# Kernel optimization log

Hardware: AMD Instinct MI355X
Metric: run time of the kernel (lower is better)

The kernel has to match this reference:

```python
import jax, jax.numpy as jnp
import numpy as np
from jax import lax

M1, M2 = 16, 16  # retained Fourier modes per spatial dim


def _spectral_conv(x, w1, w2):
    # x: [B, C, H, W] real; w1/w2: [C, C, M1, M2, 2] (re, im)
    B, C, H, W = x.shape
    xf = jnp.fft.rfft2(x, norm='ortho')            # [B, C, H, W//2+1] complex
    w1c = w1[..., 0] + 1j * w1[..., 1]
    w2c = w2[..., 0] + 1j * w2[..., 1]
    top = jnp.einsum('bixy,ioxy->boxy', xf[:, :, :M1, :M2], w1c)
    bot = jnp.einsum('bixy,ioxy->boxy', xf[:, :, -M1:, :M2], w2c)
    of = jnp.zeros((B, C, H, W // 2 + 1), dtype=xf.dtype)
    of = of.at[:, :, :M1, :M2].set(top).at[:, :, -M1:, :M2].set(bot)
    return jnp.fft.irfft2(of, s=(H, W), norm='ortho')


def _fno_block(x, w1, w2, skip_w):
    # spectral conv + linear (1x1 conv, no bias) skip
    return _spectral_conv(x, w1, w2) + jnp.einsum('bixy,io->boxy', x, skip_w)


def setup_inputs() -> dict:
    key = jax.random.key(0)
    ks = jax.random.split(key, 6)
    B, T, C, H, W = 4, 8, 64, 64, 64
    scale = 1.0 / (C * C)
    return {
        'x': jax.random.normal(ks[0], (B, T, C, H, W), dtype=jnp.float32),
        'sw1': jax.random.normal(ks[1], (6, C, C, M1, M2, 2), dtype=jnp.float32) * scale,
        'sw2': jax.random.normal(ks[2], (6, C, C, M1, M2, 2), dtype=jnp.float32) * scale,
        'skw': jax.random.normal(ks[3], (6, C, C), dtype=jnp.float32) * 0.02,
        'gate_b': jax.random.normal(ks[4], (3,), dtype=jnp.float32),
        'bias_h': jax.random.normal(ks[5], (1,), dtype=jnp.float32),
    }


def reference(x, sw1, sw2, skw, gate_b, bias_h):
    B, T, C, H, W = x.shape

    def f(i, inp):
        return _fno_block(inp, sw1[i], sw2[i], skw[i])

    def cell(xt, h):
        z = jax.nn.sigmoid(f(0, xt) + f(1, h) + gate_b[0])
        r = jax.nn.sigmoid(f(2, xt) + f(3, h) + gate_b[1])
        h_hat = jax.nn.selu(f(4, xt) + f(5, r * h) + gate_b[2])
        return (1.0 - z) * h + z * h_hat

    def step(h, xt):
        h = cell(xt, h)
        return h, None

    h0 = jnp.full((B, C, H, W), bias_h[0], dtype=x.dtype)
    h_final, _ = lax.scan(step, h0, jnp.moveaxis(x, 1, 0))  # scan over T
    return h_final  # return_sequences=False -> final hidden state [B, C, H, W]
```

## Files before the change

### kernel.cpp

```cpp
#include <hip/hip_runtime.h>

#define BB_ 4
#define TT_ 8
#define CC_ 64
#define HW 4096
#define UMAP 1024
#define STEP 0.09817477042468103f

#define OFF_UXALL 0
#define OFF_UH    (OFF_UXALL + TT_*256*UMAP)
#define OFF_URH   (OFF_UH + 256*UMAP)
#define OFF_SX    (OFF_URH + 256*UMAP)
#define OFF_SPART (OFF_SX + 3*TT_*256*UMAP)
#define OFF_H     (OFF_SPART + 2*8*256*UMAP)
#define OFF_Z     (OFF_H + BB_*CC_*HW)
#define OFF_RH    (OFF_Z + BB_*CC_*HW)
#define OFF_PH    (OFF_RH + BB_*CC_*HW)

__global__ __launch_bounds__(256) void k_init(float* __restrict__ hb,
                                              float* __restrict__ Uh,
                                              const float* __restrict__ bias_h) {
    float v = bias_h[0];
    int blk = blockIdx.x;
    if (blk < 1024) {
        int idx = (blk * 256 + threadIdx.x) * 4;
        *(float4*)(hb + idx) = make_float4(v, v, v, v);
    } else {
        int map = blk - 1024;
        float4 z = make_float4(0.f, 0.f, 0.f, 0.f);
        if (threadIdx.x == 0) z.x = 64.f * v;
        *(float4*)(Uh + (size_t)map * UMAP + threadIdx.x * 4) = z;
    }
}

__device__ __forceinline__ void dft_stages(const float* __restrict__ su,
                                           float* __restrict__ FxR, float* __restrict__ FxI,
                                           float* __restrict__ dst) {
    int tid = threadIdx.x;
    int kx = tid & 15, yb = tid >> 4;
    float stc, sts;
    __sincosf(-STEP * (float)kx, &sts, &stc);
    float wr = 1.f, wi = 0.f;
    float aR[4] = {0, 0, 0, 0}, aI[4] = {0, 0, 0, 0};
    for (int x = 0; x < 64; x++) {
        #pragma unroll
        for (int j = 0; j < 4; j++) {
            float v = su[(yb + 16 * j) * 65 + x];
            aR[j] = fmaf(v, wr, aR[j]);
            aI[j] = fmaf(v, wi, aI[j]);
        }
        float t = wr * stc - wi * sts;
        wi = wr * sts + wi * stc;
        wr = t;
    }
    #pragma unroll
    for (int j = 0; j < 4; j++) {
        FxR[(yb + 16 * j) * 16 + kx] = aR[j];
        FxI[(yb + 16 * j) * 16 + kx] = aI[j];
    }
    __syncthreads();
    int kb = tid >> 4;
    float c0, s0, c1, s1;
    __sincosf(-STEP * (float)kb, &s0, &c0);
    __sincosf(-STEP * (float)(kb + 48), &s1, &c1);
    float w0r = 1, w0i = 0, w1r = 1, w1i = 0;
    float A0r = 0, A0i = 0, A1r = 0, A1i = 0;
    for (int y = 0; y < 64; y++) {
        float Fr = FxR[y * 16 + kx], Fi = FxI[y * 16 + kx];
        A0r = fmaf(Fr, w0r, A0r); A0r = fmaf(-Fi, w0i, A0r);
        A0i = fmaf(Fr, w0i, A0i); A0i = fmaf(Fi, w0r, A0i);
        A1r = fmaf(Fr, w1r, A1r); A1r = fmaf(-Fi, w1i, A1r);
        A1i = fmaf(Fr, w1i, A1i); A1i = fmaf(Fi, w1r, A1i);
        float t0 = w0r * c0 - w0i * s0; w0i = w0r * s0 + w0i * c0; w0r = t0;
        float t1 = w1r * c1 - w1i * s1; w1i = w1r * s1 + w1i * c1; w1r = t1;
    }
    const float sc = 1.f / 64.f;
    float2* d2 = (float2*)dst;
    d2[kb * 16 + kx]        = make_float2(A0r * sc, A0i * sc);
    d2[(kb + 16) * 16 + kx] = make_float2(A1r * sc, A1i * sc);
}

__device__ __forceinline__ void dft_stages_512(const float* __restrict__ su,
                                               float* __restrict__ FxR, float* __restrict__ FxI,
                                               float* __restrict__ dst) {
    int tid = threadIdx.x;
    int kx = tid & 15, yb = tid >> 4;
    float stc, sts;
    __sincosf(-STEP * (float)kx, &sts, &stc);
    float wr = 1.f, wi = 0.f;
    float aR[2] = {0, 0}, aI[2] = {0, 0};
    for (int x = 0; x < 64; x++) {
        #pragma unroll
        for (int j = 0; j < 2; j++) {
            float v = su[(yb + 32 * j) * 65 + x];
            aR[j] = fmaf(v, wr, aR[j]);
            aI[j] = fmaf(v, wi, aI[j]);
        }
        float t = wr * stc - wi * sts;
        wi = wr * sts + wi * stc;
        wr = t;
    }
    #pragma unroll
    for (int j = 0; j < 2; j++) {
        FxR[(yb + 32 * j) * 16 + kx] = aR[j];
        FxI[(yb + 32 * j) * 16 + kx] = aI[j];
    }
    __syncthreads();
    int kb = tid >> 4;
    int ky = (kb < 16) ? kb : kb + 32;
    float c0, s0;
    __sincosf(-STEP * (float)ky, &s0, &c0);
    float w0r = 1, w0i = 0, A0r = 0, A0i = 0;
    for (int y = 0; y < 64; y++) {
        float Fr = FxR[y * 16 + kx], Fi = FxI[y * 16 + kx];
        A0r = fmaf(Fr, w0r, A0r); A0r = fmaf(-Fi, w0i, A0r);
        A0i = fmaf(Fr, w0i, A0i); A0i = fmaf(Fi, w0r, A0i);
        float t0 = w0r * c0 - w0i * s0; w0i = w0r * s0 + w0i * c0; w0r = t0;
    }
    const float sc = 1.f / 64.f;
    ((float2*)dst)[kb * 16 + kx] = make_float2(A0r * sc, A0i * sc);
}

__global__ __launch_bounds__(256) void k_dft_x(const float* __restrict__ x,
                                               float* __restrict__ Uxall) {
    __shared__ float su[64 * 65];
    __shared__ float FxR[1024], FxI[1024];
    int blk = blockIdx.x;
    int t = blk >> 8, map = blk & 255;
    int b = map >> 6, c = map & 63;
    const float* src = x + (((size_t)b * TT_ + t) * CC_ + c) * HW;
    int tid = threadIdx.x;
    #pragma unroll
    for (int k = 0; k < 4; k++) {
        int off = k * 1024 + tid * 4;
        float4 v = *(const float4*)(src + off);
        int y = off >> 6, xx = off & 63;
        su[y * 65 + xx + 0] = v.x; su[y * 65 + xx + 1] = v.y;
        su[y * 65 + xx + 2] = v.z; su[y * 65 + xx + 3] = v.w;
    }
    __syncthreads();
    dft_stages(su, FxR, FxI, Uxall + ((size_t)t * 256 + map) * UMAP);
}

__device__ __forceinline__ void mix_load(const float2* __restrict__ W2,
                                         const float2* __restrict__ U2, int i,
                                         float2 w[4], float2 u[4]) {
    const float2* wp = W2 + (size_t)i * 16384;
    const float2* up = U2 + (size_t)i * 512;
    w[0] = wp[0]; w[1] = wp[256]; w[2] = wp[512]; w[3] = wp[768];
    u[0] = up[0]; u[1] = up[32768]; u[2] = up[65536]; u[3] = up[98304];
}

__device__ __forceinline__ void mix_fma(const float2 w[4], const float2 u[4],
                                        float aR[4][4], float aI[4][4]) {
    #pragma unroll
    for (int oo = 0; oo < 4; oo++)
        #pragma unroll
        for (int bb = 0; bb < 4; bb++) {
            aR[oo][bb] = fmaf(u[bb].x, w[oo].x, aR[oo][bb]);
            aR[oo][bb] = fmaf(-u[bb].y, w[oo].y, aR[oo][bb]);
            aI[oo][bb] = fmaf(u[bb].x, w[oo].y, aI[oo][bb]);
            aI[oo][bb] = fmaf(u[bb].y, w[oo].x, aI[oo][bb]);
        }
}

__device__ __forceinline__ void mix_accum(const float2* __restrict__ W2,
                                          const float2* __restrict__ U2,
                                          int niter, float aR[4][4], float aI[4][4])
{
    float2 wA[4], uA[4], wB[4], uB[4], wN[4], uN[4];
    mix_load(W2, U2, 0, wA, uA);
    mix_load(W2, U2, 1, wB, uB);
    for (int i = 0; i + 2 < niter; i += 2) {
        mix_load(W2, U2, i + 2, wN, uN);
        mix_fma(wA, uA, aR, aI);
        #pragma unroll
        for (int k = 0; k < 4; k++) { wA[k] = wN[k]; uA[k] = uN[k]; }
        mix_load(W2, U2, i + 3, wN, uN);
        mix_fma(wB, uB, aR, aI);
        #pragma unroll
        for (int k = 0; k < 4; k++) { wB[k] = wN[k]; uB[k] = uN[k]; }
    }
    mix_fma(wA, uA, aR, aI);
    mix_fma(wB, uB, aR, aI);
}

__global__ __launch_bounds__(512, 4) void k_mix_x(
    const float* __restrict__ Uxall,
    const float* __restrict__ sw1, const float* __restrict__ sw2,
    float* __restrict__ Sx)
{
    __shared__ float2 red2[16 * 256];
    int blk = blockIdx.x;
    int mq = blk & 3;
    int tp = (blk >> 2) & 3;
    int op = (blk >> 4) & 7;
    int half = (blk >> 7) & 1;
    int li = blk >> 8;
    int l = li * 2;
    int tid = threadIdx.x;
    int kc = tid >> 8;
    int r = tid & 255;
    int ml = r & 15, og1 = (r >> 4) & 1, t1 = (r >> 5) & 1, wq = r >> 6;
    int m = mq * 64 + wq * 16 + ml;
    int o0 = (op * 2 + og1) * 4;
    int t = tp * 2 + t1;
    const float2* wt = (const float2*)(half ? sw2 : sw1);
    const float2* W2 = wt + ((size_t)(l * 4096 + o0)) * 256 + m + (size_t)kc * 32 * 16384;
    const float2* U2 = (const float2*)Uxall + (size_t)t * 131072 + half * 256 + m
                       + (size_t)kc * 32 * 512;
    float aR[4][4], aI[4][4];
    #pragma unroll
    for (int oo = 0; oo < 4; oo++)
        #pragma unroll
        for (int b = 0; b < 4; b++) { aR[oo][b] = 0.f; aI[oo][b] = 0.f; }
    #pragma unroll 4
    for (int i = 0; i < 32; ++i) {
        float2 w[4], u[4];
        mix_load(W2, U2, i, w, u);
        mix_fma(w, u, aR, aI);
    }
    if (kc) {
        #pragma unroll
        for (int oo = 0; oo < 4; oo++)
            #pragma unroll
            for (int b = 0; b < 4; b++)
                red2[(oo * 4 + b) * 256 + r] = make_float2(aR[oo][b], aI[oo][b]);
    }
    __syncthreads();
    if (kc == 0) {
        float2* S2 = (float2*)Sx;
        #pragma unroll
        for (int oo = 0; oo < 4; oo++)
            #pragma unroll
            for (int b = 0; b < 4; b++) {
                float2 p = red2[(oo * 4 + b) * 256 + r];
                S2[((size_t)(li * 8 + t) * 256 + b * 64 + o0 + oo) * 512 + half * 256 + m]
                    = make_float2(aR[oo][b] + p.x, aI[oo][b] + p.y);
            }
    }
}

__device__ __forceinline__ void mix_body_h(int blk, int l0, int l1,
    const float* __restrict__ U,
    const float* __restrict__ sw1, const float* __restrict__ sw2,
    float* __restrict__ Spart)
{
    int og = blk & 15;
    int ic = (blk >> 4) & 7;
    int half = (blk >> 7) & 1;
    int g = (blk >> 8) & 1;
    int m = threadIdx.x;
    int o0 = og * 4, ib = ic * 8;
    int l = g ? l1 : l0;
    const float2* wt = (const float2*)(half ? sw2 : sw1);
    const float2* W2 = wt + (((size_t)l * 64 + ib) * 64 + o0) * 256 + m;
    const float2* U2 = (const float2*)U + (size_t)ib * 512 + half * 256 + m;
    float aR[4][4], aI[4][4];
    #pragma unroll
    for (int oo = 0; oo < 4; oo++)
        #pragma unroll
        for (int b = 0; b < 4; b++) { aR[oo][b] = 0.f; aI[oo][b] = 0.f; }
    mix_accum(W2, U2, 8, aR, aI);
    float2* S2 = (float2*)Spart;
    #pragma unroll
    for (int oo = 0; oo < 4; oo++)
        #pragma unroll
        for (int b = 0; b < 4; b++)
            S2[((size_t)(g * 8 + ic) * 256 + b * 64 + o0 + oo) * 512 + half * 256 + m]
                = make_float2(aR[oo][b], aI[oo][b]);
}

__device__ __forceinline__ void fma16(const float4 w, const float4 u, float acc[4][4]) {
    acc[0][0] = fmaf(u.x, w.x, acc[0][0]); acc[0][1] = fmaf(u.y, w.x, acc[0][1]);
    acc[0][2] = fmaf(u.z, w.x, acc[0][2]); acc[0][3] = fmaf(u.w, w.x, acc[0][3]);
    acc[1][0] = fmaf(u.x, w.y, acc[1][0]); acc[1][1] = fmaf(u.y, w.y, acc[1][1]);
    acc[1][2] = fmaf(u.z, w.y, acc[1][2]); acc[1][3] = fmaf(u.w, w.y, acc[1][3]);
    acc[2][0] = fmaf(u.x, w.z, acc[2][0]); acc[2][1] = fmaf(u.y, w.z, acc[2][1]);
    acc[2][2] = fmaf(u.z, w.z, acc[2][2]); acc[2][3] = fmaf(u.w, w.z, acc[2][3]);
    acc[3][0] = fmaf(u.x, w.w, acc[3][0]); acc[3][1] = fmaf(u.y, w.w, acc[3][1]);
    acc[3][2] = fmaf(u.z, w.w, acc[3][2]); acc[3][3] = fmaf(u.w, w.w, acc[3][3]);
}

__device__ __forceinline__ void skip_gemm(int rr, float* __restrict__ sW,
    const float* __restrict__ uA, long long bsA,
    const float* __restrict__ uB, long long bsB,
    const float* __restrict__ skw, int lA, int lB, float gb,
    float* __restrict__ out)
{
    int pxc = rr & 31, oh = (rr >> 5) & 1, b = rr >> 6;
    int tid = threadIdx.x;
    int ot = tid & 7, pt = tid >> 3;
    #pragma unroll
    for (int n = 0; n < 4; n++) {
        int idx = n * 1024 + tid * 4;
        int k = idx >> 5, oc = idx & 31;
        int p = k >> 6, i = k & 63;
        *(float4*)(sW + idx) =
            *(const float4*)(skw + (p ? lB : lA) * 4096 + i * 64 + oh * 32 + oc);
    }
    __syncthreads();
    float acc[4][4];
    #pragma unroll
    for (int oo = 0; oo < 4; oo++)
        #pragma unroll
        for (int q = 0; q < 4; q++) acc[oo][q] = 0.f;
    const float* pa = uA + (long long)b * bsA + pxc * 128 + pt * 4;
    const float* pb = uB + (long long)b * bsB + pxc * 128 + pt * 4;
    const float4* sW4 = (const float4*)sW;
    #pragma unroll 4
    for (int i = 0; i < 64; i++) {
        float4 ua = *(const float4*)(pa + (size_t)i * HW);
        float4 wa = sW4[i * 8 + ot];
        fma16(wa, ua, acc);
        float4 ub = *(const float4*)(pb + (size_t)i * HW);
        float4 wb = sW4[(64 + i) * 8 + ot];
        fma16(wb, ub, acc);
    }
    float* op = out + ((long long)(b * 64 + oh * 32 + ot * 4)) * HW + pxc * 128 + pt * 4;
    #pragma unroll
    for (int oo = 0; oo < 4; oo++) {
        float4 r = make_float4(acc[oo][0] + gb, acc[oo][1] + gb,
                               acc[oo][2] + gb, acc[oo][3] + gb);
        *(float4*)(op + (size_t)oo * HW) = r;
    }
}

__global__ __launch_bounds__(256) void k_front_zr(
    const float* __restrict__ Uh,
    const float* __restrict__ xt, const float* __restrict__ hb,
    const float* __restrict__ sw1, const float* __restrict__ sw2,
    const float* __restrict__ skw, const float* __restrict__ gate_b,
    float* __restrict__ Spart, float* __restrict__ zb, float* __restrict__ rhb)
{
    __shared__ float smem[4096];
    int blk = blockIdx.x;
    if (blk < 512) {
        mix_body_h(blk, 1, 3, Uh, sw1, sw2, Spart);
    } else {
        int r = blk - 512;
        int g = r >> 8;
        skip_gemm(r & 255, smem,
                  xt, (long long)TT_ * CC_ * HW, hb, (long long)CC_ * HW,
                  skw, g ? 2 : 0, g ? 3 : 1, gate_b[g], g ? rhb : zb);
    }
}

__global__ __launch_bounds__(256) void k_front_h(
    const float* __restrict__ Urh,
    const float* __restrict__ xt, const float* __restrict__ rhb,
    const float* __restrict__ sw1, const float* __restrict__ sw2,
    const float* __restrict__ skw, const float* __restrict__ gate_b,
    float* __restrict__ Spart, float* __restrict__ phb)
{
    __shared__ float smem[4096];
    int blk = blockIdx.x;
    if (blk < 256) {
        mix_body_h(blk, 5, 5, Urh, sw1, sw2, Spart);
    } else {
        int r = blk - 256;
        skip_gemm(r, smem,
                  xt, (long long)TT_ * CC_ * HW, rhb, (long long)CC_ * HW,
                  skw, 4, 5, gate_b[2], phb);
    }
}

__device__ __forceinline__ void idft_stage1_512(const float* __restrict__ SR,
                                                const float* __restrict__ SI,
                                                float* __restrict__ GR, float* __restrict__ GI)
{
    int tid = threadIdx.x;
    int kx = tid & 15, yb = tid >> 4;
    #pragma unroll
    for (int j = 0; j < 2; j++) {
        int y = yb + 32 * j;
        float stc, sts;
        __sincosf(STEP * (float)y, &sts, &stc);
        float ar = 0.f, ai = 0.f;
        float wr = 1.f, wi = 0.f;
        for (int k = 0; k < 16; k++) {
            float sr_ = SR[k * 16 + kx], si_ = SI[k * 16 + kx];
            ar = fmaf(sr_, wr, ar); ar = fmaf(-si_, wi, ar);
            ai = fmaf(sr_, wi, ai); ai = fmaf(si_, wr, ai);
            float t = wr * stc - wi * sts; wi = wr * sts + wi * stc; wr = t;
        }
        int q = (3 * y) & 3;
        float w2r = (q == 0) ? 1.f : ((q == 2) ? -1.f : 0.f);
        float w2i = (q == 1) ? 1.f : ((q == 3) ? -1.f : 0.f);
        for (int k = 16; k < 32; k++) {
            float sr_ = SR[k * 16 + kx], si_ = SI[k * 16 + kx];
            ar = fmaf(sr_, w2r, ar); ar = fmaf(-si_, w2i, ar);
            ai = fmaf(sr_, w2i, ai); ai = fmaf(si_, w2r, ai);
            float t = w2r * stc - w2i * sts; w2i = w2r * sts + w2i * stc; w2r = t;
        }
        GR[y * 16 + kx] = ar;
        GI[y * 16 + kx] = ai;
    }
}

__global__ __launch_bounds__(512) void k_back_zr(
    const float* __restrict__ Spart, const float* __restrict__ Sx, int t,
    float* __restrict__ zb, float* __restrict__ rhb,
    const float* __restrict__ hb, float* __restrict__ Urh)
{
    __shared__ float smem[6208];
    float* SR = smem;
    float* SI = smem + 512;
    float* GR = smem + 1024;
    float* GI = smem + 2048;
    int g = blockIdx.x >> 8;
    int map = blockIdx.x & 255;
    int tid = threadIdx.x;
    {
        float2 v = ((const float2*)Sx)[((size_t)(g * 8 + t) * 256 + map) * 512 + tid];
        float sr = v.x, si = v.y;
        const float2* base = (const float2*)Spart;
        #pragma unroll
        for (int ic = 0; ic < 8; ic++) {
            float2 p = base[((size_t)(g * 8 + ic) * 256 + map) * 512 + tid];
            sr += p.x; si += p.y;
        }
        SR[tid] = sr; SI[tid] = si;
    }
    __syncthreads();
    idft_stage1_512(SR, SI, GR, GI);
    __syncthreads();
    int x = tid & 63, ybase = tid >> 6;
    float cx, sx;
    __sincosf(STEP * (float)x, &sx, &cx);
    size_t mo = (size_t)map * HW;
    float rhv[8];
    #pragma unroll
    for (int j = 0; j < 8; j++) {
        int y = ybase + 8 * j;
        float acc = GR[y * 16];
        float wr = cx, wi = sx;
        #pragma unroll
        for (int k = 1; k < 16; k++) {
            acc = fmaf(2.f * GR[y * 16 + k], wr, acc);
            acc = fmaf(-2.f * GI[y * 16 + k], wi, acc);
            float t2 = wr * cx - wi * sx; wi = wr * sx + wi * cx; wr = t2;
        }
        float val = acc * (1.f / 64.f);
        int idx = y * 64 + x;
        if (g == 0) {
            float pre = val + zb[mo + idx];
            zb[mo + idx] = 1.f / (1.f + __expf(-pre));
        } else {
            float pre = val + rhb[mo + idx];
            float rr = 1.f / (1.f + __expf(-pre));
            float rh = rr * hb[mo + idx];
            rhb[mo + idx] = rh;
            rhv[j] = rh;
        }
    }
    if (g == 0) return;
    __syncthreads();
    float* su = smem;
    #pragma unroll
    for (int j = 0; j < 8; j++) {
        int y = ybase + 8 * j;
        su[y * 65 + x] = rhv[j];
    }
    __syncthreads();
    dft_stages_512(su, smem + 4160, smem + 5184, Urh + (size_t)map * UMAP);
}

__global__ __launch_bounds__(512) void k_back_h(
    const float* __restrict__ Spart, const float* __restrict__ Sx, int t,
    const float* __restrict__ zb, const float* __restrict__ phb,
    float* __restrict__ hb, float* __restrict__ Uh)
{
    __shared__ float smem[6208];
    float* SR = smem;
    float* SI = smem + 512;
    float* GR = smem + 1024;
    float* GI = smem + 2048;
    int map = blockIdx.x & 255;
    int tid = threadIdx.x;
    {
        float2 v = ((const float2*)Sx)[((size_t)(2 * 8 + t) * 256 + map) * 512 + tid];
        float sr = v.x, si = v.y;
        const float2* base = (const float2*)Spart;
        #pragma unroll
        for (int ic = 0; ic < 8; ic++) {
            float2 p = base[((size_t)ic * 256 + map) * 512 + tid];
            sr += p.x; si += p.y;
        }
        SR[tid] = sr; SI[tid] = si;
    }
    __syncthreads();
    idft_stage1_512(SR, SI, GR, GI);
    __syncthreads();
    int x = tid & 63, ybase = tid >> 6;
    float cx, sx;
    __sincosf(STEP * (float)x, &sx, &cx);
    size_t mo = (size_t)map * HW;
    float hv[8];
    #pragma unroll
    for (int j = 0; j < 8; j++) {
        int y = ybase + 8 * j;
        float acc = GR[y * 16];
        float wr = cx, wi = sx;
        #pragma unroll
        for (int k = 1; k < 16; k++) {
            acc = fmaf(2.f * GR[y * 16 + k], wr, acc);
            acc = fmaf(-2.f * GI[y * 16 + k], wi, acc);
            float t2 = wr * cx - wi * sx; wi = wr * sx + wi * cx; wr = t2;
        }
        float val = acc * (1.f / 64.f);
        int idx = y * 64 + x;
        float pre = val + phb[mo + idx];
        float hh = (pre > 0.f) ? 1.0507009873554805f * pre
                               : 1.7580993408473766f * (__expf(pre) - 1.f);
        float z = zb[mo + idx];
        float hn = fmaf(z, hh - hb[mo + idx], hb[mo + idx]);
        hb[mo + idx] = hn;
        hv[j] = hn;
    }
    __syncthreads();
    float* su = smem;
    #pragma unroll
    for (int j = 0; j < 8; j++) {
        int y = ybase + 8 * j;
        su[y * 65 + x] = hv[j];
    }
    __syncthreads();
    dft_stages_512(su, smem + 4160, smem + 5184, Uh + (size_t)map * UMAP);
}

extern "C" void kernel_launch(void* const* d_in, const int* in_sizes, int n_in,
                              void* d_out, int out_size, void* d_ws, size_t ws_size,
                              hipStream_t stream)
{
    (void)in_sizes; (void)n_in; (void)out_size; (void)ws_size;
    const float* x   = (const float*)d_in[0];
    const float* sw1 = (const float*)d_in[1];
    const float* sw2 = (const float*)d_in[2];
    const float* skw = (const float*)d_in[3];
    const float* gb  = (const float*)d_in[4];
    const float* bh  = (const float*)d_in[5];
    float* ws    = (float*)d_ws;
    float* Uxall = ws + OFF_UXALL;
    float* Uh    = ws + OFF_UH;
    float* Urh   = ws + OFF_URH;
    float* Sx    = ws + OFF_SX;
    float* Sp    = ws + OFF_SPART;
    float* hb    = ws + OFF_H;
    float* zb    = ws + OFF_Z;
    float* rhb   = ws + OFF_RH;
    float* phb   = ws + OFF_PH;

    k_init<<<1280, 256, 0, stream>>>(hb, Uh, bh);
    k_dft_x<<<2048, 256, 0, stream>>>(x, Uxall);
    k_mix_x<<<768, 512, 0, stream>>>(Uxall, sw1, sw2, Sx);
    for (int t = 0; t < TT_; t++) {
        const float* xt = x + (size_t)t * CC_ * HW;
        k_front_zr<<<1024, 256, 0, stream>>>(Uh, xt, hb, sw1, sw2, skw, gb,
                                             Sp, zb, rhb);
        k_back_zr<<<512, 512, 0, stream>>>(Sp, Sx, t, zb, rhb, hb, Urh);
        k_front_h<<<512, 256, 0, stream>>>(Urh, xt, rhb, sw1, sw2, skw, gb,
                                           Sp, phb);
        k_back_h<<<256, 512, 0, stream>>>(Sp, Sx, t, zb, phb, hb, Uh);
    }
    hipMemcpyAsync(d_out, hb, (size_t)BB_ * CC_ * HW * sizeof(float),
                   hipMemcpyDeviceToDevice, stream);
}
```

Measured before the change: 787.2 us.

## Restructure k_mix_x into LDS-tiled double-buffered complex GEMM

Rewrites the x-side spectral mixing kernel so each 256-thread block stages weight and Fourier-coefficient tiles in shared memory with double buffering and register prefetch. Each thread then computes 8 outputs by 2 time-batch pairs from LDS. This replaces the earlier split-K scheme that used direct global loads and a shared-memory reduction. The goal is more reuse of the weights across all timesteps and batches per load, at the cost of two barriers per chunk and more LDS traffic.

```diff
diff --git a/kernel.cpp b/kernel.cpp
--- a/kernel.cpp
+++ b/kernel.cpp
@@ -185,60 +185,96 @@
     mix_fma(wB, uB, aR, aI);
 }
 
-__global__ __launch_bounds__(512, 4) void k_mix_x(
+__global__ __launch_bounds__(256, 4) void k_mix_x(
     const float* __restrict__ Uxall,
     const float* __restrict__ sw1, const float* __restrict__ sw2,
     float* __restrict__ Sx)
 {
-    __shared__ float2 red2[16 * 256];
+    __shared__ float4 Wt4[2][256];
+    __shared__ float4 Ut4[2][1024];
     int blk = blockIdx.x;
-    int mq = blk & 3;
-    int tp = (blk >> 2) & 3;
+    int mq = blk & 15;
     int op = (blk >> 4) & 7;
     int half = (blk >> 7) & 1;
     int li = blk >> 8;
     int l = li * 2;
     int tid = threadIdx.x;
-    int kc = tid >> 8;
-    int r = tid & 255;
-    int ml = r & 15, og1 = (r >> 4) & 1, t1 = (r >> 5) & 1, wq = r >> 6;
-    int m = mq * 64 + wq * 16 + ml;
-    int o0 = (op * 2 + og1) * 4;
-    int t = tp * 2 + t1;
-    const float2* wt = (const float2*)(half ? sw2 : sw1);
-    const float2* W2 = wt + ((size_t)(l * 4096 + o0)) * 256 + m + (size_t)kc * 32 * 16384;
-    const float2* U2 = (const float2*)Uxall + (size_t)t * 131072 + half * 256 + m
-                       + (size_t)kc * 32 * 512;
-    float aR[4][4], aI[4][4];
-    #pragma unroll
-    for (int oo = 0; oo < 4; oo++)
-        #pragma unroll
-        for (int b = 0; b < 4; b++) { aR[oo][b] = 0.f; aI[oo][b] = 0.f; }
-    #pragma unroll 4
-    for (int i = 0; i < 32; ++i) {
-        float2 w[4], u[4];
-        mix_load(W2, U2, i, w, u);
-        mix_fma(w, u, aR, aI);
-    }
-    if (kc) {
-        #pragma unroll
-        for (int oo = 0; oo < 4; oo++)
+    int m0 = mq * 16;
+    int o0 = op * 8;
+    const float2* wsrc = (const float2*)(half ? sw2 : sw1);
+    const float2* usrc = (const float2*)Uxall;
+
+    int wl = tid & 7;
+    int wrow = tid >> 3;
+    int wii = wrow >> 3, woo = wrow & 7;
+    const float4* wg4 = (const float4*)(wsrc
+        + (((size_t)(l * 64 + wii) * 64) + o0 + woo) * 256 + m0) + wl;
+    int ut_ = wrow >> 2, ub_ = wrow & 3;
+    const float4* ug4 = (const float4*)(usrc
+        + (size_t)ut_ * 131072 + (size_t)ub_ * 32768 + half * 256 + m0) + wl;
+
+    int mt = tid & 15, pp = tid >> 4;
+    float aR[8][2], aI[8][2];
+    #pragma unroll
+    for (int oo = 0; oo < 8; oo++) {
+        aR[oo][0] = 0.f; aR[oo][1] = 0.f;
+        aI[oo][0] = 0.f; aI[oo][1] = 0.f;
+    }
+
+    float4 wv  = wg4[0];
+    float4 uv0 = ug4[0];
+    float4 uv1 = ug4[256];
+    float4 uv2 = ug4[512];
+    float4 uv3 = ug4[768];
+
+    for (int c = 0; c < 16; ++c) {
+        int cb = c & 1;
+        Wt4[cb][tid] = wv;
+        Ut4[cb][tid] = uv0;
+        Ut4[cb][256 + tid] = uv1;
+        Ut4[cb][512 + tid] = uv2;
+        Ut4[cb][768 + tid] = uv3;
+        if (c < 15) {
+            size_t ib = (size_t)(c + 1) * 4;
+            wv  = wg4[ib * 8192];
+            uv0 = ug4[ib * 256];
+            uv1 = ug4[(ib + 1) * 256];
+            uv2 = ug4[(ib + 2) * 256];
+            uv3 = ug4[(ib + 3) * 256];
+        }
+        __syncthreads();
+        const float2* Wl = (const float2*)Wt4[cb];
+        const float2* Ul = (const float2*)Ut4[cb];
+        #pragma unroll
+        for (int ii = 0; ii < 4; ii++) {
+            float2 u0 = Ul[(ii * 32 + 2 * pp) * 16 + mt];
+            float2 u1 = Ul[(ii * 32 + 2 * pp + 1) * 16 + mt];
             #pragma unroll
-            for (int b = 0; b < 4; b++)
-                red2[(oo * 4 + b) * 256 + r] = make_float2(aR[oo][b], aI[oo][b]);
-    }
-    __syncthreads();
-    if (kc == 0) {
-        float2* S2 = (float2*)Sx;
-        #pragma unroll
-        for (int oo = 0; oo < 4; oo++)
-            #pragma unroll
-            for (int b = 0; b < 4; b++) {
-                float2 p = red2[(oo * 4 + b) * 256 + r];
-                S2[((size_t)(li * 8 + t) * 256 + b * 64 + o0 + oo) * 512 + half * 256 + m]
-                    = make_float2(aR[oo][b] + p.x, aI[oo][b] + p.y);
+            for (int oo = 0; oo < 8; oo++) {
+                float2 w = Wl[(ii * 8 + oo) * 16 + mt];
+                aR[oo][0] = fmaf(u0.x, w.x, aR[oo][0]);
+                aR[oo][0] = fmaf(-u0.y, w.y, aR[oo][0]);
+                aI[oo][0] = fmaf(u0.x, w.y, aI[oo][0]);
+                aI[oo][0] = fmaf(u0.y, w.x, aI[oo][0]);
+                aR[oo][1] = fmaf(u1.x, w.x, aR[oo][1]);
+                aR[oo][1] = fmaf(-u1.y, w.y, aR[oo][1]);
+                aI[oo][1] = fmaf(u1.x, w.y, aI[oo][1]);
+                aI[oo][1] = fmaf(u1.y, w.x, aI[oo][1]);
             }
-    }
+        }
+        __syncthreads();
+    }
+
+    float2* S2 = (float2*)Sx;
+    #pragma unroll
+    for (int oo = 0; oo < 8; oo++)
+        #pragma unroll
+        for (int j = 0; j < 2; j++) {
+            int tb = 2 * pp + j;
+            int t = tb >> 2, b = tb & 3;
+            S2[((size_t)(li * 8 + t) * 256 + b * 64 + o0 + oo) * 512
+               + half * 256 + m0 + mt] = make_float2(aR[oo][j], aI[oo][j]);
+        }
 }
 
 __device__ __forceinline__ void mix_body_h(int blk, int l0, int l1,
@@ -553,7 +589,7 @@
 
     k_init<<<1280, 256, 0, stream>>>(hb, Uh, bh);
     k_dft_x<<<2048, 256, 0, stream>>>(x, Uxall);
-    k_mix_x<<<768, 512, 0, stream>>>(Uxall, sw1, sw2, Sx);
+    k_mix_x<<<768, 256, 0, stream>>>(Uxall, sw1, sw2, Sx);
     for (int t = 0; t < TT_; t++) {
         const float* xt = x + (size_t)t * CC_ * HW;
         k_front_zr<<<1024, 256, 0, stream>>>(Uh, xt, hb, sw1, sw2, skw, gb,
```

Measured after the change: 748.4 us. 4.9% less time.
